# Performance work log

Measured on AMD Instinct MI355X. Metric: run time of the kernel, lower is better.

The kernel has to match this reference:

```python
import jax, jax.numpy as jnp
import numpy as np

B, N = 2, 6
H, W = 64, 64            # BEV grid
FH, FW = 32, 88          # camera feature map
DIM, FEAT_DIM = 128, 128
HEADS, DH = 4, 32
QW1, QW2 = 8, 8          # query window
KW1, KW2 = 4, 11         # key/val window
IMG_H, IMG_W = 224, 480
EPS = 1e-5


def _ln(t, g, b):
    m = t.mean(-1, keepdims=True)
    v = ((t - m) ** 2).mean(-1, keepdims=True)
    return (t - m) / jnp.sqrt(v + EPS) * g + b


def _bn_relu_conv(t, g, b, Wc):
    # eval-mode BatchNorm2d (running_mean=0, running_var=1) -> ReLU -> 1x1 conv
    y = jax.nn.relu(t / jnp.sqrt(1.0 + EPS) * g[:, None, None] + b[:, None, None])
    return jnp.einsum('oc,nchw->nohw', Wc, y)


def _normalize(t, axis):
    n = jnp.sqrt(jnp.sum(t * t, axis=axis, keepdims=True))
    return t / jnp.maximum(n, 1e-12)


def _win(t, w1, w2):
    # (..., X*w1, Y*w2, d) -> (..., X, Y, w1, w2, d)
    s = t.shape
    t = t.reshape(*s[:-3], s[-3] // w1, w1, s[-2] // w2, w2, s[-1])
    return jnp.swapaxes(t, -4, -3)


def _unwin(t):
    # (..., X, Y, w1, w2, d) -> (..., X*w1, Y*w2, d)
    s = t.shape
    return jnp.swapaxes(t, -4, -3).reshape(*s[:-5], s[-5] * s[-3], s[-4] * s[-2], s[-1])


def _gridwin(t, w1, w2):
    bb, nn, Ht, Wt, d = t.shape
    t = t.reshape(bb, nn, w1, Ht // w1, w2, Wt // w2, d)
    return t.transpose(0, 1, 3, 5, 2, 4, 6)  # (b, n, X, Y, w1, w2, d)


def _cross_win_attn(qw, kw, vw, ln_g, ln_b, Wqkv, bqkv, Wp, bp, skip):
    b, n, X, Y, w1, w2, d = qw.shape
    f1, f2 = kw.shape[4], kw.shape[5]
    L = X * Y
    q = qw.transpose(0, 2, 3, 1, 4, 5, 6).reshape(b, L, n * w1 * w2, d)
    k = kw.transpose(0, 2, 3, 1, 4, 5, 6).reshape(b, L, n * f1 * f2, d)
    v = vw.transpose(0, 2, 3, 1, 4, 5, 6).reshape(b, L, n * f1 * f2, d)
    q = _ln(q, ln_g[0], ln_b[0]) @ Wqkv[0] + bqkv[0]
    k = _ln(k, ln_g[1], ln_b[1]) @ Wqkv[1] + bqkv[1]
    v = _ln(v, ln_g[2], ln_b[2]) @ Wqkv[2] + bqkv[2]
    split = lambda t: t.reshape(*t.shape[:-1], HEADS, DH)  # head-major channel split
    q, k, v = split(q), split(k), split(v)
    att = jax.nn.softmax(DH ** -0.5 * jnp.einsum('blqhd,blkhd->bhlqk', q, k), axis=-1)
    o = jnp.einsum('bhlqk,blkhd->blqhd', att, v).reshape(b, L, n * w1 * w2, HEADS * DH)
    o = o @ Wp + bp
    o = o.reshape(b, X, Y, n, w1, w2, d).mean(3)  # mean over cameras
    return o + skip


def _forward(x, grid, feature, I_inv, E_inv,
             bn_fl_g, bn_fl_b, W_fl, bn_fp_g, bn_fp_b, W_fp,
             W_bev, b_bev, W_img, W_cam,
             attn_ln_g, attn_ln_b, attn_Wqkv, attn_bqkv, attn_Wp, attn_bp,
             pn_g, pn_b, Wma, bma, Wmb, bmb, post_g, post_b):
    b, n = feature.shape[:2]
    # image plane (buffer)
    xs = jnp.linspace(0.0, 1.0, FW) * IMG_W
    ys = jnp.linspace(0.0, 1.0, FH) * IMG_H
    gx, gy = jnp.meshgrid(xs, ys)  # (FH, FW) each
    plane = jnp.stack([gx, gy, jnp.ones_like(gx)], 0).reshape(3, FH * FW)
    # camera embedding from translation column of E_inv
    c = E_inv[..., -1]                                   # (b, n, 4)
    c_embed = jnp.einsum('oc,bnc->bno', W_cam, c)        # (b, n, dim)
    # unprojected rays
    cam = jnp.einsum('bnij,jk->bnik', I_inv, plane)      # (b, n, 3, HW)
    cam = jnp.concatenate([cam, jnp.ones_like(cam[:, :, :1])], 2)
    d = jnp.einsum('bnij,bnjk->bnik', E_inv, cam)        # (b, n, 4, HW)
    d_img = d.reshape(b, n, 4, FH, FW)
    d_embed = jnp.einsum('oc,bnchw->bnohw', W_img, d_img)
    img_embed = _normalize(d_embed - c_embed[..., None, None], axis=2)
    # BEV positional embedding
    w_embed = jnp.einsum('oc,chw->ohw', W_bev, grid[:2]) + b_bev[:, None, None]
    bev_embed = _normalize(w_embed[None, None] - c_embed[..., None, None], axis=2)  # (b,n,dim,H,W)
    feat = feature.reshape(b * n, FEAT_DIM, FH, FW)
    key_im = img_embed + _bn_relu_conv(feat, bn_fp_g, bn_fp_b, W_fp).reshape(b, n, DIM, FH, FW)
    val_im = _bn_relu_conv(feat, bn_fl_g, bn_fl_b, W_fl).reshape(b, n, DIM, FH, FW)
    query = bev_embed + x[:, None]                       # (b, n, dim, H, W)
    # channel-last
    q_im = query.transpose(0, 1, 3, 4, 2)
    k_im = key_im.transpose(0, 1, 3, 4, 2)
    v_im = val_im.transpose(0, 1, 3, 4, 2)
    x_im = x.transpose(0, 2, 3, 1)
    # stage 1: local windows
    qw = _win(q_im, QW1, QW2)
    kw = _win(k_im, KW1, KW2)
    vw = _win(v_im, KW1, KW2)
    o1 = _cross_win_attn(qw, kw, vw, attn_ln_g[0], attn_ln_b[0], attn_Wqkv[0],
                         attn_bqkv[0], attn_Wp[0], attn_bp[0], _win(x_im, QW1, QW2))
    q1 = _unwin(o1)                                      # (b, H, W, d)
    q1 = q1 + jax.nn.gelu(_ln(q1, pn_g[0], pn_b[0]) @ Wma[0] + bma[0], approximate=False) @ Wmb[0] + bmb[0]
    # stage 2: grid (swapped) windows
    qg = jnp.broadcast_to(q1[:, None], (b, n) + q1.shape[1:])
    o2 = _cross_win_attn(_win(qg, QW1, QW2), _gridwin(k_im, KW1, KW2), _gridwin(v_im, KW1, KW2),
                         attn_ln_g[1], attn_ln_b[1], attn_Wqkv[1], attn_bqkv[1],
                         attn_Wp[1], attn_bp[1], _win(q1, QW1, QW2))
    q2 = _unwin(o2)
    q2 = q2 + jax.nn.gelu(_ln(q2, pn_g[1], pn_b[1]) @ Wma[1] + bma[1], approximate=False) @ Wmb[1] + bmb[1]
    out = _ln(q2, post_g, post_b)
    return out.transpose(0, 3, 1, 2)                     # (b, dim, H, W)


def setup_inputs() -> dict:
    key = jax.random.key(0)
    ks = jax.random.split(key, 16)
    rn = lambda i, shape, sc=0.02: jax.random.normal(ks[i], shape, dtype=jnp.float32) * sc
    return {
        'index': 0,
        'x': jax.random.normal(ks[0], (B, DIM, H, W), dtype=jnp.float32),
        'grid': jax.random.normal(ks[1], (2, H, W), dtype=jnp.float32),
        'feature': jax.random.normal(ks[2], (B, N, FEAT_DIM, FH, FW), dtype=jnp.float32),
        'I_inv': jax.random.normal(ks[3], (B, N, 3, 3), dtype=jnp.float32),
        'E_inv': jax.random.normal(ks[4], (B, N, 4, 4), dtype=jnp.float32),
        'bn_fl_g': jnp.ones((FEAT_DIM,), jnp.float32), 'bn_fl_b': jnp.zeros((FEAT_DIM,), jnp.float32),
        'W_fl': rn(5, (DIM, FEAT_DIM)),
        'bn_fp_g': jnp.ones((FEAT_DIM,), jnp.float32), 'bn_fp_b': jnp.zeros((FEAT_DIM,), jnp.float32),
        'W_fp': rn(6, (DIM, FEAT_DIM)),
        'W_bev': rn(7, (DIM, 2)), 'b_bev': jnp.zeros((DIM,), jnp.float32),
        'W_img': rn(8, (DIM, 4)), 'W_cam': rn(9, (DIM, 4)),
        'attn_ln_g': jnp.ones((2, 3, DIM), jnp.float32), 'attn_ln_b': jnp.zeros((2, 3, DIM), jnp.float32),
        'attn_Wqkv': rn(10, (2, 3, DIM, HEADS * DH)), 'attn_bqkv': jnp.zeros((2, 3, HEADS * DH), jnp.float32),
        'attn_Wp': rn(11, (2, HEADS * DH, DIM)), 'attn_bp': jnp.zeros((2, DIM), jnp.float32),
        'pn_g': jnp.ones((2, DIM), jnp.float32), 'pn_b': jnp.zeros((2, DIM), jnp.float32),
        'Wma': rn(12, (2, DIM, 2 * DIM)), 'bma': jnp.zeros((2, 2 * DIM), jnp.float32),
        'Wmb': rn(13, (2, 2 * DIM, DIM)), 'bmb': jnp.zeros((2, DIM), jnp.float32),
        'post_g': jnp.ones((DIM,), jnp.float32), 'post_b': jnp.zeros((DIM,), jnp.float32),
    }


def reference(index, x, grid, feature, I_inv, E_inv,
              bn_fl_g, bn_fl_b, W_fl, bn_fp_g, bn_fp_b, W_fp,
              W_bev, b_bev, W_img, W_cam,
              attn_ln_g, attn_ln_b, attn_Wqkv, attn_bqkv, attn_Wp, attn_bp,
              pn_g, pn_b, Wma, bma, Wmb, bmb, post_g, post_b):
    del index  # grid for this index is passed directly
    return _forward(x, grid, feature, I_inv, E_inv,
                    bn_fl_g, bn_fl_b, W_fl, bn_fp_g, bn_fp_b, W_fp,
                    W_bev, b_bev, W_img, W_cam,
                    attn_ln_g, attn_ln_b, attn_Wqkv, attn_bqkv, attn_Wp, attn_bp,
                    pn_g, pn_b, Wma, bma, Wmb, bmb, post_g, post_b)
```

## Files before the change

### kernel.cpp

```cpp
#include <hip/hip_runtime.h>
#include <math.h>


typedef __attribute__((ext_vector_type(8))) short short8;
typedef __attribute__((ext_vector_type(4))) float f32x4;

__device__ __forceinline__ unsigned short f2bf(float f){
  union { float f; unsigned u; } v; v.f = f;
  unsigned r = v.u + 0x7FFF + ((v.u >> 16) & 1);
  return (unsigned short)(r >> 16);
}
__device__ __forceinline__ float bf2f(unsigned short h){
  union { unsigned u; float f; } v; v.u = ((unsigned)h) << 16; return v.f;
}
__device__ __forceinline__ void store_bf16x8(unsigned short* p, const float* v){
  union { short8 s8; unsigned short u[8]; } u;
  #pragma unroll
  for (int i=0;i<8;i++) u.u[i] = f2bf(v[i]);
  *(short8*)p = u.s8;
}

__device__ __forceinline__ float gelu_erf(float x){
  float z = x * 0.70710678118654752f;
  float a = fabsf(z);
  float t = 1.0f / fmaf(0.3275911f, a, 1.0f);
  float p = t*(0.254829592f + t*(-0.284496736f + t*(1.421413741f +
            t*(-1.453152027f + t*1.061405429f))));
  float er = 1.0f - p*__expf(-a*a);
  er = copysignf(er, z);
  return 0.5f * x * (1.0f + er);
}

__device__ __forceinline__ size_t remap_kv(int tok, int mode){
  int bn = tok / 2816; int p = tok - bn*2816;
  int b = bn / 6, n = bn - b*6;
  int i = p / 88, j = p - i*88;
  int l, t;
  if (mode == 1){
    int jw = j / 11;
    l = (i >> 2)*8 + jw;
    t = n*44 + (i & 3)*11 + (j - jw*11);
  } else {
    l = (i & 7)*8 + (j & 7);
    t = n*44 + (i >> 3)*11 + (j >> 3);
  }
  return (size_t)((b*64 + l)*264 + t);
}

__global__ __launch_bounds__(128) void k_prep(
    const float* __restrict__ qkv, const float* __restrict__ wp,
    const float* __restrict__ wma, const float* __restrict__ wmb,
    const float* __restrict__ wfl, const float* __restrict__ wfp,
    unsigned short* __restrict__ Wt,
    const float* __restrict__ Iinv, const float* __restrict__ Einv,
    const float* __restrict__ Wimg, const float* __restrict__ Wcam,
    unsigned short* __restrict__ K1h,
    const float* __restrict__ gridp, const float* __restrict__ Wbev,
    const float* __restrict__ bbev, const float* __restrict__ x,
    const float* __restrict__ lg, const float* __restrict__ lb,
    const float* __restrict__ abqkv, float* __restrict__ biasP,
    unsigned short* __restrict__ Qh){
  __shared__ float sx[128][9];
  int bid = blockIdx.x;
  if (bid < 64){
    const int sel[16]  = {0,0,0,0,0,0, 1,1, 2,2, 3,3,3,3, 4,5};
    const int soff[16] = {0,16384,32768,49152,65536,81920, 0,16384, 0,32768,
                          0,16384,32768,49152, 0,0};
    const int doff[16] = {0,16384,32768,49152,65536,81920, 98304,114688,
                          131072,163840, 196608,212992,229376,245760, 262144,278528};
    const int Ns[16]   = {128,128,128,128,128,128, 128,128, 256,256,
                          128,128,128,128, 128,128};
    const int trs[16]  = {1,1,1,1,1,1, 1,1, 1,1, 1,1,1,1, 0,0};
    int sg = bid >> 2, q = bid & 3;
    const float* srcs[6] = {qkv, wp, wma, wmb, wfl, wfp};
    const float* src = srcs[sel[sg]] + soff[sg];
    unsigned short* dst = Wt + doff[sg];
    int K = 128, N = Ns[sg];
    int quarter = (K*N) >> 2;
    bool fold = (sg >= 1 && sg <= 5);
    const float* gv = lg + sg*128;
    for (int idx = q*quarter + threadIdx.x; idx < (q+1)*quarter; idx += 128){
      int n = idx / K, k = idx - n*K;
      float v = trs[sg] ? src[k*N + n] : src[idx];
      if (fold) v *= gv[k];
      dst[idx] = f2bf(v);
    }
  } else if (bid < 70){
    int m = bid - 64;
    int n = threadIdx.x;
    float s = abqkv[m*128 + n];
    if (m > 0){
      const float* lnb = lb + m*128;
      const float* W = qkv + m*16384;
      for (int k=0;k<128;k++) s = fmaf(lnb[k], W[k*128 + n], s);
    }
    biasP[m*128 + n] = s;
  } else if (bid < 4294){
    int tile = bid - 70;
    int bn = tile / 352; int p0 = (tile - bn*352)*8;
    int xid = threadIdx.x >> 4, part = threadIdx.x & 15;
    int p = p0 + xid;
    int i = p / 88, j = p - i*88;
    float xs = (float)j * (480.0f/87.0f);
    float ys = (float)i * (224.0f/31.0f);
    const float* I = Iinv + bn*9;
    const float* E = Einv + bn*16;
    float c0 = I[0]*xs + I[1]*ys + I[2];
    float c1 = I[3]*xs + I[4]*ys + I[5];
    float c2 = I[6]*xs + I[7]*ys + I[8];
    float d0 = E[0]*c0 + E[1]*c1 + E[2]*c2 + E[3];
    float d1 = E[4]*c0 + E[5]*c1 + E[6]*c2 + E[7];
    float d2 = E[8]*c0 + E[9]*c1 + E[10]*c2 + E[11];
    float d3 = E[12]*c0 + E[13]*c1 + E[14]*c2 + E[15];
    float v[8]; float sq = 0.f;
    #pragma unroll
    for (int k=0;k<8;k++){
      int o = part*8 + k;
      const float* W = Wimg + o*4;
      const float* Wc = Wcam + o*4;
      float de = W[0]*d0 + W[1]*d1 + W[2]*d2 + W[3]*d3;
      float ce = Wc[0]*E[3] + Wc[1]*E[7] + Wc[2]*E[11] + Wc[3]*E[15];
      float vv = de - ce;
      v[k] = vv; sq = fmaf(vv, vv, sq);
    }
    #pragma unroll
    for (int off=8; off>0; off>>=1) sq += __shfl_xor(sq, off, 16);
    float rn = 1.0f / fmaxf(sqrtf(sq), 1e-12f);
    float o8[8];
    #pragma unroll
    for (int k=0;k<8;k++) o8[k] = v[k]*rn;
    store_bf16x8(K1h + (size_t)(bn*2816 + p)*128 + part*8, o8);
  } else {
    int bid2 = bid - 4294;
    int b = bid2 >> 9; int pp0 = (bid2 & 511) << 3;
    {
      int cg = threadIdx.x >> 3, px = threadIdx.x & 7;
      #pragma unroll
      for (int i=0;i<8;i++){
        int c = cg + 16*i;
        sx[c][px] = x[(size_t)b*524288 + (size_t)c*4096 + pp0 + px];
      }
    }
    __syncthreads();
    int xid = threadIdx.x >> 4, part = threadIdx.x & 15;
    int pix = pp0 + xid;
    int h = pix >> 6, w = pix & 63;
    int l = (h>>3)*8 + (w>>3);
    int tq = (h&7)*8 + (w&7);
    float g0 = gridp[pix], g1 = gridp[4096 + pix];
    float we[8], xv[8];
    #pragma unroll
    for (int k=0;k<8;k++){
      int o = part*8 + k;
      we[k] = Wbev[o*2]*g0 + Wbev[o*2+1]*g1 + bbev[o];
      xv[k] = sx[part*8+k][xid];
    }
    for (int n=0; n<6; n++){
      const float* E = Einv + (b*6+n)*16;
      float v[8]; float sq = 0.f;
      #pragma unroll
      for (int k=0;k<8;k++){
        int o = part*8 + k;
        const float* Wc = Wcam + o*4;
        float ce = Wc[0]*E[3] + Wc[1]*E[7] + Wc[2]*E[11] + Wc[3]*E[15];
        float vv = we[k] - ce;
        v[k] = vv; sq = fmaf(vv, vv, sq);
      }
      #pragma unroll
      for (int off=8; off>0; off>>=1) sq += __shfl_xor(sq, off, 16);
      float rn = 1.0f / fmaxf(sqrtf(sq), 1e-12f);
      float q[8]; float s=0.f, s2=0.f;
      #pragma unroll
      for (int k=0;k<8;k++){
        q[k] = fmaf(v[k], rn, xv[k]);
        s += q[k]; s2 = fmaf(q[k], q[k], s2);
      }
      #pragma unroll
      for (int off=8; off>0; off>>=1){ s += __shfl_xor(s, off, 16); s2 += __shfl_xor(s2, off, 16); }
      float mean = s*(1.f/128.f);
      float rstd = rsqrtf(fmaxf(s2*(1.f/128.f) - mean*mean, 0.f) + 1e-5f);
      size_t row = (size_t)((b*64 + l)*384 + n*64 + tq);
      float o8[8];
      #pragma unroll
      for (int k=0;k<8;k++){
        int c = part*8 + k;
        o8[k] = fmaf((q[k]-mean)*rstd, lg[c], lb[c]);
      }
      store_bf16x8(Qh + row*128 + part*8, o8);
    }
  }
}

__global__ __launch_bounds__(256) void k_conv(const float* __restrict__ feat,
    const float* __restrict__ gK, const float* __restrict__ bK,
    const unsigned short* __restrict__ WK, unsigned short* __restrict__ K1h,
    const float* __restrict__ gV, const float* __restrict__ bV,
    const unsigned short* __restrict__ WV, unsigned short* __restrict__ V1h){
  constexpr int KP_ = 136;
  __shared__ unsigned short sW[128*KP_];
  __shared__ unsigned short sA[128*KP_];
  __shared__ float sg[128], sb[128];
  __shared__ float sMean[128], sRstd[128];
  const int which = (blockIdx.x >= 264);
  const int bid = which ? blockIdx.x - 264 : blockIdx.x;
  const float* gg = which ? gV : gK;
  const float* bb = which ? bV : bK;
  const unsigned short* Wts = which ? WV : WK;
  unsigned short* OUT = which ? V1h : K1h;
  const int tid = threadIdx.x;
  const int base = bid * 128;
  for (int i = tid; i < 2048; i += 256){
    int n = i >> 4, k8 = (i & 15) << 3;
    *(short8*)&sW[n*KP_ + k8] = *(const short8*)(Wts + (size_t)n*128 + k8);
  }
  if (tid < 128){ sg[tid]=gg[tid]; sb[tid]=bb[tid]; }
  const float RSQ = rsqrtf(1.0f + 1e-5f);
  {
    int prow = tid & 127, cseg = tid >> 7;
    int bn = base / 2816;
    int p = base - bn*2816 + prow;
    const float* fb = feat + ((size_t)bn*128 + cseg*64)*2816 + p;
    #pragma unroll 8
    for (int i=0;i<64;i+=2){
      int c = cseg*64 + i;
      float t0 = fb[(size_t)i*2816] * RSQ;
      float t1 = fb[(size_t)(i+1)*2816] * RSQ;
      float y0 = fmaxf(fmaf(t0, sg[c],   sb[c]),   0.f);
      float y1 = fmaxf(fmaf(t1, sg[c+1], sb[c+1]), 0.f);
      unsigned u = (unsigned)f2bf(y0) | ((unsigned)f2bf(y1) << 16);
      *(unsigned*)&sA[prow*KP_ + c] = u;
    }
  }
  __syncthreads();
  const int lane = tid & 63, wv = tid >> 6;
  const int lane15 = lane & 15, quad = lane >> 4;
  const int n0 = wv * 32;
  f32x4 acc[8][2];
  #pragma unroll
  for (int mt=0; mt<8; mt++){ acc[mt][0]=(f32x4)0.f; acc[mt][1]=(f32x4)0.f; }
  const unsigned short* aptr = sA + lane15*KP_ + quad*8;
  const unsigned short* bptr = sW + (size_t)(n0 + lane15)*KP_ + quad*8;
  #pragma unroll
  for (int kk=0; kk<4; kk++){
    short8 af[8], bf2v[2];
    #pragma unroll
    for (int mt=0; mt<8; mt++) af[mt] = *(const short8*)(aptr + mt*16*KP_ + kk*32);
    bf2v[0] = *(const short8*)(bptr + kk*32);
    bf2v[1] = *(const short8*)(bptr + 16*KP_ + kk*32);
    #pragma unroll
    for (int mt=0; mt<8; mt++){
      acc[mt][0] = __builtin_amdgcn_mfma_f32_16x16x32_bf16(af[mt], bf2v[0], acc[mt][0], 0,0,0);
      acc[mt][1] = __builtin_amdgcn_mfma_f32_16x16x32_bf16(af[mt], bf2v[1], acc[mt][1], 0,0,0);
    }
  }
  __syncthreads();
  #pragma unroll
  for (int mt=0; mt<8; mt++){
    #pragma unroll
    for (int nt=0; nt<2; nt++){
      int col = n0 + nt*16 + lane15;
      #pragma unroll
      for (int r4=0; r4<4; r4++){
        int row = mt*16 + quad*4 + r4;
        float v = acc[mt][nt][r4];
        if (!which) v += bf2f(K1h[(size_t)(base+row)*128 + col]);
        sA[row*KP_ + col] = f2bf(v);
      }
    }
  }
  __syncthreads();
  {
    int r = tid >> 1, part = tid & 1;
    float s=0.f, s2=0.f;
    #pragma unroll 8
    for (int k=0;k<64;k++){
      float v = bf2f(sA[r*KP_ + part*64 + k]);
      s += v; s2 = fmaf(v,v,s2);
    }
    s += __shfl_xor(s, 1); s2 += __shfl_xor(s2, 1);
    if (part == 0){
      float mean = s*(1.f/128.f);
      sMean[r] = mean;
      sRstd[r] = rsqrtf(fmaxf(s2*(1.f/128.f) - mean*mean, 0.f) + 1e-5f);
    }
  }
  __syncthreads();
  for (int i = tid; i < 2048; i += 256){
    int row = i >> 4, seg = i & 15;
    float mean = sMean[row], rstd = sRstd[row];
    union { short8 s; unsigned short u[8]; } t;
    t.s = *(const short8*)&sA[row*KP_ + seg*8];
    float v[8];
    #pragma unroll
    for (int k=0;k<8;k++) v[k] = (bf2f(t.u[k]) - mean)*rstd;
    store_bf16x8(OUT + (size_t)(base+row)*128 + seg*8, v);
  }
}

struct GArg {
  const unsigned short* Xh;
  const unsigned short* Wt; const float* bias;
  unsigned short* OUTH; float oscale; int outmode;
};
struct G5 { GArg g[5]; int s[4]; };

__global__ __launch_bounds__(256) void k_qkv5(G5 A){
  constexpr int KP_ = 136;
  __shared__ unsigned short sW[128*KP_];
  __shared__ unsigned short sA[128*KP_];
  __shared__ float sbias[128];
  const int b0 = (int)blockIdx.x;
  const int ridx = (b0 < A.s[0]) ? 0 : (b0 < A.s[1]) ? 1 : (b0 < A.s[2]) ? 2
                 : (b0 < A.s[3]) ? 3 : 4;
  const GArg g = A.g[ridx];
  const int bid = b0 - (ridx ? A.s[ridx-1] : 0);
  const int base = bid * 128;
  const int tid = threadIdx.x;
  for (int i = tid; i < 2048; i += 256){
    int n = i >> 4, k8 = (i & 15) << 3;
    *(short8*)&sW[n*KP_ + k8] = *(const short8*)(g.Wt + (size_t)n*128 + k8);
  }
  if (tid < 128) sbias[tid] = g.bias[tid];
  {
    const int r = tid >> 1, part = tid & 1;
    const short8* src = (const short8*)(g.Xh + (size_t)(base+r)*128 + part*64);
    short8* dst = (short8*)(sA + r*KP_ + part*64);
    #pragma unroll
    for (int k=0;k<8;k++) dst[k] = src[k];
// ... 15 lines not shown
    bf2v[0] = *(const short8*)(bptr + kk*32);
    bf2v[1] = *(const short8*)(bptr + 16*KP_ + kk*32);
    #pragma unroll
    for (int mt=0; mt<8; mt++){
      acc[mt][0] = __builtin_amdgcn_mfma_f32_16x16x32_bf16(af[mt], bf2v[0], acc[mt][0], 0,0,0);
      acc[mt][1] = __builtin_amdgcn_mfma_f32_16x16x32_bf16(af[mt], bf2v[1], acc[mt][1], 0,0,0);
    }
  }
  __syncthreads();
  #pragma unroll
  for (int mt=0; mt<8; mt++){
    #pragma unroll
    for (int nt=0; nt<2; nt++){
      int col = n0 + nt*16 + lane15;
      float bsv = sbias[col];
      #pragma unroll
      for (int r4=0; r4<4; r4++){
        int row = mt*16 + quad*4 + r4;
        sA[row*KP_ + col] = f2bf((acc[mt][nt][r4] + bsv) * g.oscale);
      }
    }
  }
  __syncthreads();
  for (int i = tid; i < 2048; i += 256){
    int row = i >> 4, seg = i & 15;
    int rrow = base + row;
    size_t orow = g.outmode ? remap_kv(rrow, g.outmode) : (size_t)rrow;
    *(short8*)(g.OUTH + orow*128 + seg*8) = *(const short8*)&sA[row*KP_ + seg*8];
  }
}

__global__ __launch_bounds__(256) void k_tail(
    const unsigned short* __restrict__ AOh,
    const float* __restrict__ skipf, int skipmode,
    const unsigned short* __restrict__ WtP, const float* __restrict__ abp,
    const float* __restrict__ png, const float* __restrict__ pnb,
    const unsigned short* __restrict__ WtMAa, const unsigned short* __restrict__ WtMAb,
    const float* __restrict__ bma,
    const unsigned short* __restrict__ WtMBa, const unsigned short* __restrict__ WtMBb,
    const float* __restrict__ bmb,
    float* __restrict__ Q1out,
    const unsigned short* __restrict__ WtQ2, const float* __restrict__ q2bias,
    float q2scale, unsigned short* __restrict__ QPout,
    const float* __restrict__ postg, const float* __restrict__ postb,
    float* __restrict__ out){
  constexpr int KP_ = 136;
  __shared__ unsigned short sW[128*KP_];
  __shared__ unsigned short sX[32*KP_];
  __shared__ unsigned short sH1[32*KP_];
  __shared__ unsigned short sH2[32*KP_];
  __shared__ float sCUR[32*132];
  __shared__ float sbias[128];
  __shared__ float sg[128], sb2[128];
  __shared__ float sMean[32], sRstd[32];
  const int tid = threadIdx.x;
  const int base = blockIdx.x * 32;
  const int lane = tid & 63, wv = tid >> 6;
  const int lane15 = lane & 15, quad = lane >> 4;
  const int n0 = wv * 32;

  auto loadW = [&](const unsigned short* Wp){
    for (int i = tid; i < 2048; i += 256){
      int n = i >> 4, k8 = (i & 15) << 3;
      *(short8*)&sW[n*KP_ + k8] = *(const short8*)(Wp + (size_t)n*128 + k8);
    }
  };
  auto domfma = [&](const unsigned short* Asrc, f32x4 acc[2][2]){
    const unsigned short* aptr = Asrc + lane15*KP_ + quad*8;
    const unsigned short* bptr = sW + (size_t)(n0 + lane15)*KP_ + quad*8;
    #pragma unroll
    for (int kk=0; kk<4; kk++){
      short8 a0 = *(const short8*)(aptr + kk*32);
      short8 a1 = *(const short8*)(aptr + 16*KP_ + kk*32);
      short8 b0 = *(const short8*)(bptr + kk*32);
      short8 b1 = *(const short8*)(bptr + 16*KP_ + kk*32);
      acc[0][0] = __builtin_amdgcn_mfma_f32_16x16x32_bf16(a0,b0,acc[0][0],0,0,0);
      acc[1][0] = __builtin_amdgcn_mfma_f32_16x16x32_bf16(a1,b0,acc[1][0],0,0,0);
      acc[0][1] = __builtin_amdgcn_mfma_f32_16x16x32_bf16(a0,b1,acc[0][1],0,0,0);
      acc[1][1] = __builtin_amdgcn_mfma_f32_16x16x32_bf16(a1,b1,acc[1][1],0,0,0);
    }
  };

  loadW(WtP);
  {
    const int r = tid >> 3, part = tid & 7;
    const short8* src = (const short8*)(AOh + (size_t)(base+r)*128 + part*16);
    short8* dst = (short8*)(sX + r*KP_ + part*16);
    dst[0] = src[0]; dst[1] = src[1];
  }
  if (tid < 128){ sbias[tid] = abp[tid]; sg[tid] = png[tid]; sb2[tid] = pnb[tid]; }
  __syncthreads();
  {
    f32x4 acc[2][2];
    acc[0][0]=(f32x4)0.f; acc[0][1]=(f32x4)0.f;
    acc[1][0]=(f32x4)0.f; acc[1][1]=(f32x4)0.f;
    domfma(sX, acc);
    #pragma unroll
    for (int mt=0; mt<2; mt++)
      #pragma unroll
      for (int nt=0; nt<2; nt++){
        int col = n0 + nt*16 + lane15;
        float bsv = sbias[col];
        #pragma unroll
        for (int r4=0; r4<4; r4++){
          int row = mt*16 + quad*4 + r4;
          int rrow = base + row;
          float v = acc[mt][nt][r4] + bsv;
          if (skipmode == 1){
            int bb = rrow >> 12, l = (rrow >> 6) & 63, pp = rrow & 63;
            int pix = (((l>>3)*8 + (pp>>3)) << 6) + (l&7)*8 + (pp&7);
            v += skipf[(size_t)bb*524288 + (size_t)col*4096 + pix];
          } else {
            v += skipf[(size_t)rrow*128 + col];
          }
          sCUR[row*132 + col] = v;
        }
      }
// ... 179 lines not shown
      for (int off=4; off>0; off>>=1){ s += __shfl_xor(s, off, 8); s2 += __shfl_xor(s2, off, 8); }
      if (part == 0){
        float mean = s*(1.f/128.f);
        sMean[r] = mean;
        sRstd[r] = rsqrtf(fmaxf(s2*(1.f/128.f) - mean*mean, 0.f) + 1e-5f);
      }
    }
    __syncthreads();
    {
      int c = tid & 127, half = tid >> 7;
      int b = base >> 12, l = (base >> 6) & 63, p0 = base & 63;
      float go = postg[c], bo = postb[c];
      #pragma unroll
      for (int seg=0; seg<2; seg++){
        int p = p0 + half*16 + seg*8;
        int hrow = (l>>3)*8 + (p>>3);
        int w0 = (l&7)*8;
        float rr[8];
        #pragma unroll
        for (int j=0;j<8;j++){
          int row = half*16 + seg*8 + j;
          rr[j] = fmaf((sCUR[row*132 + c] - sMean[row])*sRstd[row], go, bo);
        }
        size_t obase = ((size_t)(b*128 + c))*4096 + (size_t)hrow*64 + w0;
        *(float4*)&out[obase]   = make_float4(rr[0],rr[1],rr[2],rr[3]);
        *(float4*)&out[obase+4] = make_float4(rr[4],rr[5],rr[6],rr[7]);
      }
    }
  }
}

__global__ __launch_bounds__(256) void k_attn2(const unsigned short* __restrict__ QPh,
    const unsigned short* __restrict__ KPh, const unsigned short* __restrict__ VPh,
    unsigned short* __restrict__ AOh, int nrep, int nQ){
  __shared__ unsigned short Ksh[288*40];
  __shared__ unsigned short Vt[32*296];
  __shared__ unsigned short Psh[4*16*40];
  __shared__ float rs[4*16];
  int hd = blockIdx.x & 3; int bl = blockIdx.x >> 2;
  size_t kvbase = (size_t)bl*264;
  int tid = threadIdx.x;
  for (int idx = tid; idx < 1056; idx += 256){
    int row = idx >> 2, seg = idx & 3;
    *(short8*)&Ksh[row*40 + seg*8] =
      *(const short8*)(KPh + (kvbase+row)*128 + hd*32 + seg*8);
  }
  for (int idx = tid; idx < 96; idx += 256){
    int row = 264 + (idx>>2), seg = idx & 3;
    short8 z = {0,0,0,0,0,0,0,0};
    *(short8*)&Ksh[row*40 + seg*8] = z;
  }
  for (int idx = tid; idx < 528; idx += 256){
    int kp = idx >> 2, seg = idx & 3;
    union { short8 s; unsigned short u[8]; } a, b;
    a.s = *(const short8*)(VPh + (kvbase + 2*kp)*128 + hd*32 + seg*8);
    b.s = *(const short8*)(VPh + (kvbase + 2*kp + 1)*128 + hd*32 + seg*8);
    #pragma unroll
    for (int i=0;i<8;i++)
      *(unsigned*)&Vt[(seg*8+i)*296 + 2*kp] = (unsigned)a.u[i] | ((unsigned)b.u[i] << 16);
  }
  for (int idx = tid; idx < 384; idx += 256){
    int d = idx / 12, kp = 264 + (idx % 12)*2;
    *(unsigned*)&Vt[d*296 + kp] = 0u;
  }
  __syncthreads();
  const int wv = tid >> 6, lane = tid & 63;
  const int lane15 = lane & 15, quad = lane >> 4;
  unsigned short* Pw = Psh + wv*640;
  float* rsw = rs + wv*16;
  short8 vfrag[9][2];
  #pragma unroll
  for (int kc=0; kc<9; kc++){
    vfrag[kc][0] = *(const short8*)&Vt[(lane15)*296      + kc*32 + quad*8];
    vfrag[kc][1] = *(const short8*)&Vt[(16+lane15)*296   + kc*32 + quad*8];
  }
  f32x4 macc0 = (f32x4)0.f, macc1 = (f32x4)0.f;
  for (int cam = 0; cam < nrep; cam++){
    int qrow = bl*nQ + (cam*4 + wv)*16 + lane15;
    short8 qf = *(const short8*)(QPh + (size_t)qrow*128 + hd*32 + quad*8);
    f32x4 oa0 = (f32x4)0.f, oa1 = (f32x4)0.f;
    float rsum = 0.f;
    #pragma unroll
    for (int kc=0; kc<9; kc++){
      #pragma unroll
      for (int sub=0; sub<2; sub++){
        int kt = kc*2 + sub;
        short8 kf = *(const short8*)&Ksh[(kt*16 + lane15)*40 + quad*8];
        f32x4 st = __builtin_amdgcn_mfma_f32_16x16x32_bf16(kf, qf, (f32x4)0.f, 0,0,0);
        int kbase = kt*16 + quad*4;
        float e0 = (kbase+0 < 264) ? __expf(st[0]) : 0.f;
        float e1 = (kbase+1 < 264) ? __expf(st[1]) : 0.f;
        float e2 = (kbase+2 < 264) ? __expf(st[2]) : 0.f;
        float e3 = (kbase+3 < 264) ? __expf(st[3]) : 0.f;
        rsum += (e0+e1)+(e2+e3);
        uint2 pk;
        pk.x = (unsigned)f2bf(e0) | ((unsigned)f2bf(e1) << 16);
        pk.y = (unsigned)f2bf(e2) | ((unsigned)f2bf(e3) << 16);
        *(uint2*)&Pw[lane15*40 + sub*16 + quad*4] = pk;
      }
      short8 pf = *(const short8*)&Pw[lane15*40 + quad*8];
      oa0 = __builtin_amdgcn_mfma_f32_16x16x32_bf16(pf, vfrag[kc][0], oa0, 0,0,0);
      oa1 = __builtin_amdgcn_mfma_f32_16x16x32_bf16(pf, vfrag[kc][1], oa1, 0,0,0);
    }
    rsum += __shfl_xor(rsum, 16);
    rsum += __shfl_xor(rsum, 32);
    if (lane < 16) rsw[lane] = rsum;
    f32x4 rv = *(f32x4*)&rsw[quad*4];
    #pragma unroll
    for (int r=0;r<4;r++){
      float inv = 1.f / rv[r];
      macc0[r] = fmaf(oa0[r], inv, macc0[r]);
      macc1[r] = fmaf(oa1[r], inv, macc1[r]);
    }
  }
  float sc = (nrep == 6) ? (1.f/6.f) : 1.f;
  int pixb = wv*16 + quad*4;
  #pragma unroll
  for (int r=0;r<4;r++){
    size_t rowo = ((size_t)(bl*64 + pixb + r))*128 + hd*32;
    AOh[rowo + lane15]      = f2bf(macc0[r]*sc);
    AOh[rowo + 16 + lane15] = f2bf(macc1[r]*sc);
  }
}

extern "C" void kernel_launch(void* const* d_in, const int* in_sizes, int n_in,
                              void* d_out, int out_size, void* d_ws, size_t ws_size,
                              hipStream_t stream) {
  (void)in_sizes; (void)n_in; (void)out_size; (void)ws_size;
  const float* x     = (const float*)d_in[1];
  const float* gridp = (const float*)d_in[2];
  const float* feat  = (const float*)d_in[3];
  const float* Iinv  = (const float*)d_in[4];
  const float* Einv  = (const float*)d_in[5];
  const float* gfl   = (const float*)d_in[6];
  const float* bfl   = (const float*)d_in[7];
  const float* Wfl   = (const float*)d_in[8];
  const float* gfp   = (const float*)d_in[9];
  const float* bfp   = (const float*)d_in[10];
  const float* Wfp   = (const float*)d_in[11];
  const float* Wbev  = (const float*)d_in[12];
  const float* bbev  = (const float*)d_in[13];
  const float* Wimg  = (const float*)d_in[14];
  const float* Wcam  = (const float*)d_in[15];
  const float* alng  = (const float*)d_in[16];
  const float* alnb  = (const float*)d_in[17];
  const float* aWqkv = (const float*)d_in[18];
  const float* abqkv = (const float*)d_in[19];
  const float* aWp   = (const float*)d_in[20];
  const float* abp   = (const float*)d_in[21];
  const float* png   = (const float*)d_in[22];
  const float* pnb   = (const float*)d_in[23];
  const float* Wma   = (const float*)d_in[24];
  const float* bma   = (const float*)d_in[25];
  const float* Wmb   = (const float*)d_in[26];
  const float* bmb   = (const float*)d_in[27];
  const float* postg = (const float*)d_in[28];
  const float* postb = (const float*)d_in[29];
  float* out = (float*)d_out;
  float* ws  = (float*)d_ws;
  const float QSC = 0.17677669529663687f;

  float* biasP = ws;
  unsigned short* Wt   = (unsigned short*)(ws + 2048);
  unsigned short* K1h  = (unsigned short*)(ws + 149504);
  unsigned short* V1h  = K1h + 4325376;
  unsigned short* KPh  = V1h + 4325376;
  unsigned short* VPh  = KPh + 4325376;
  unsigned short* KP2h = VPh + 4325376;
  unsigned short* VP2h = KP2h + 4325376;
  unsigned short* QPh  = VP2h + 4325376;
  unsigned short* Qbh  = QPh + 6291456;
  unsigned short* AOh  = Qbh + 6291456;
  float* Q1f = (float*)(AOh + 1048576);

  unsigned short* WtQ1 = Wt;            unsigned short* WtK1 = Wt + 16384;
  unsigned short* WtV1 = Wt + 32768;    unsigned short* WtQ2 = Wt + 49152;
  unsigned short* WtK2 = Wt + 65536;    unsigned short* WtV2 = Wt + 81920;
  unsigned short* WtP1 = Wt + 98304;    unsigned short* WtP2 = Wt + 114688;
  unsigned short* WtMA1 = Wt + 131072;  unsigned short* WtMA2 = Wt + 163840;
  unsigned short* WtMB1a = Wt + 196608; unsigned short* WtMB1b = Wt + 212992;
  unsigned short* WtMB2a = Wt + 229376; unsigned short* WtMB2b = Wt + 245760;
  unsigned short* WtFL = Wt + 262144;   unsigned short* WtFP = Wt + 278528;

  k_prep<<<5318, 128, 0, stream>>>(aWqkv, aWp, Wma, Wmb, Wfl, Wfp, Wt,
      Iinv, Einv, Wimg, Wcam, K1h, gridp, Wbev, bbev, x, alng, alnb,
      abqkv, biasP, Qbh);

  k_conv<<<528, 256, 0, stream>>>(feat, gfp, bfp, WtFP, K1h,
                                  gfl, bfl, WtFL, V1h);

  {
    G5 A;
    A.g[0] = GArg{Qbh, WtQ1, biasP,      QPh,  QSC, 0};
    A.g[1] = GArg{K1h, WtK1, biasP+128,  KPh,  1.f, 1};
    A.g[2] = GArg{V1h, WtV1, biasP+256,  VPh,  1.f, 1};
    A.g[3] = GArg{K1h, WtK2, biasP+512,  KP2h, 1.f, 2};
    A.g[4] = GArg{V1h, WtV2, biasP+640,  VP2h, 1.f, 2};
    A.s[0] = 384; A.s[1] = 648; A.s[2] = 912; A.s[3] = 1176;
    k_qkv5<<<1440, 256, 0, stream>>>(A);
  }
  k_attn2<<<512, 256, 0, stream>>>(QPh, KPh, VPh, AOh, 6, 384);
  k_tail<<<256, 256, 0, stream>>>(AOh, x, 1, WtP1, abp, png, pnb,
      WtMA1, WtMA1+16384, bma, WtMB1a, WtMB1b, bmb, Q1f,
      WtQ2, biasP+384, QSC, QPh,
      nullptr, nullptr, nullptr);
  k_attn2<<<512, 256, 0, stream>>>(QPh, KP2h, VP2h, AOh, 1, 64);
  k_tail<<<256, 256, 0, stream>>>(AOh, Q1f, 3, WtP2, abp+128, png+128, pnb+128,
      WtMA2, WtMA2+16384, bma+256, WtMB2a, WtMB2b, bmb+128, nullptr,
      nullptr, nullptr, 0.f, nullptr,
      postg, postb, out);
}
```

Before: 273.5 us.

## Split first cross-attention over camera groups with fp32 partials reduced in tail

The first attention launch is split into three camera groups of two cameras each, tripling the grid from 512 to 1536 blocks. Each group writes fp32 partial outputs to a new workspace buffer, and the first tail kernel sums the three partials before converting them to bf16. This targets low occupancy in the first attention pass, where only 512 blocks each looped over six cameras. In exchange, every group reloads the K/V tile into shared memory and writes extra fp32 traffic that the tail must read back.

```diff
diff --git a/kernel.cpp b/kernel.cpp
--- a/kernel.cpp
+++ b/kernel.cpp
@@ -375,6 +375,7 @@
 
 __global__ __launch_bounds__(256) void k_tail(
     const unsigned short* __restrict__ AOh,
+    const float* __restrict__ AOf3,
     const float* __restrict__ skipf, int skipmode,
     const unsigned short* __restrict__ WtP, const float* __restrict__ abp,
     const float* __restrict__ png, const float* __restrict__ pnb,
@@ -425,7 +426,16 @@
   };
 
   loadW(WtP);
-  {
+  if (AOf3){
+    const int r = tid >> 3, part = tid & 7;
+    const float* p0 = AOf3 + (size_t)(base+r)*128 + part*16;
+    float v[16];
+    #pragma unroll
+    for (int k=0;k<16;k++)
+      v[k] = p0[k] + p0[1048576 + k] + p0[2097152 + k];
+    store_bf16x8(sX + r*KP_ + part*16, v);
+    store_bf16x8(sX + r*KP_ + part*16 + 8, v+8);
+  } else {
     const int r = tid >> 3, part = tid & 7;
     const short8* src = (const short8*)(AOh + (size_t)(base+r)*128 + part*16);
     short8* dst = (short8*)(sX + r*KP_ + part*16);
@@ -671,12 +681,15 @@
 
 __global__ __launch_bounds__(256) void k_attn2(const unsigned short* __restrict__ QPh,
     const unsigned short* __restrict__ KPh, const unsigned short* __restrict__ VPh,
-    unsigned short* __restrict__ AOh, int nrep, int nQ){
+    unsigned short* __restrict__ AOh, float* __restrict__ AOf,
+    int ncam, int nQ, float osc){
   __shared__ unsigned short Ksh[288*40];
   __shared__ unsigned short Vt[32*296];
   __shared__ unsigned short Psh[4*16*40];
   __shared__ float rs[4*16];
-  int hd = blockIdx.x & 3; int bl = blockIdx.x >> 2;
+  int hd = blockIdx.x & 3; int bl = (blockIdx.x >> 2) & 127;
+  int cp = blockIdx.x >> 9;
+  int cam0 = cp * ncam;
   size_t kvbase = (size_t)bl*264;
   int tid = threadIdx.x;
   for (int idx = tid; idx < 1056; idx += 256){
@@ -714,7 +727,8 @@
     vfrag[kc][1] = *(const short8*)&Vt[(16+lane15)*296   + kc*32 + quad*8];
   }
   f32x4 macc0 = (f32x4)0.f, macc1 = (f32x4)0.f;
-  for (int cam = 0; cam < nrep; cam++){
+  for (int ci = 0; ci < ncam; ci++){
+    int cam = cam0 + ci;
     int qrow = bl*nQ + (cam*4 + wv)*16 + lane15;
     short8 qf = *(const short8*)(QPh + (size_t)qrow*128 + hd*32 + quad*8);
     f32x4 oa0 = (f32x4)0.f, oa1 = (f32x4)0.f;
@@ -752,13 +766,21 @@
       macc1[r] = fmaf(oa1[r], inv, macc1[r]);
     }
   }
-  float sc = (nrep == 6) ? (1.f/6.f) : 1.f;
   int pixb = wv*16 + quad*4;
-  #pragma unroll
-  for (int r=0;r<4;r++){
-    size_t rowo = ((size_t)(bl*64 + pixb + r))*128 + hd*32;
-    AOh[rowo + lane15]      = f2bf(macc0[r]*sc);
-    AOh[rowo + 16 + lane15] = f2bf(macc1[r]*sc);
+  if (AOf){
+    #pragma unroll
+    for (int r=0;r<4;r++){
+      size_t rowo = ((size_t)(cp*8192 + bl*64 + pixb + r))*128 + hd*32;
+      AOf[rowo + lane15]      = macc0[r]*osc;
+      AOf[rowo + 16 + lane15] = macc1[r]*osc;
+    }
+  } else {
+    #pragma unroll
+    for (int r=0;r<4;r++){
+      size_t rowo = ((size_t)(bl*64 + pixb + r))*128 + hd*32;
+      AOh[rowo + lane15]      = f2bf(macc0[r]*osc);
+      AOh[rowo + 16 + lane15] = f2bf(macc1[r]*osc);
+    }
   }
 }
 
@@ -811,6 +833,7 @@
   unsigned short* Qbh  = QPh + 6291456;
   unsigned short* AOh  = Qbh + 6291456;
   float* Q1f = (float*)(AOh + 1048576);
+  float* AOf = Q1f + 1048576;
 
   unsigned short* WtQ1 = Wt;            unsigned short* WtK1 = Wt + 16384;
   unsigned short* WtV1 = Wt + 32768;    unsigned short* WtQ2 = Wt + 49152;
@@ -838,13 +861,13 @@
     A.s[0] = 384; A.s[1] = 648; A.s[2] = 912; A.s[3] = 1176;
     k_qkv5<<<1440, 256, 0, stream>>>(A);
   }
-  k_attn2<<<512, 256, 0, stream>>>(QPh, KPh, VPh, AOh, 6, 384);
-  k_tail<<<256, 256, 0, stream>>>(AOh, x, 1, WtP1, abp, png, pnb,
+  k_attn2<<<1536, 256, 0, stream>>>(QPh, KPh, VPh, nullptr, AOf, 2, 384, 1.f/6.f);
+  k_tail<<<256, 256, 0, stream>>>(nullptr, AOf, x, 1, WtP1, abp, png, pnb,
       WtMA1, WtMA1+16384, bma, WtMB1a, WtMB1b, bmb, Q1f,
       WtQ2, biasP+384, QSC, QPh,
       nullptr, nullptr, nullptr);
-  k_attn2<<<512, 256, 0, stream>>>(QPh, KP2h, VP2h, AOh, 1, 64);
-  k_tail<<<256, 256, 0, stream>>>(AOh, Q1f, 3, WtP2, abp+128, png+128, pnb+128,
+  k_attn2<<<512, 256, 0, stream>>>(QPh, KP2h, VP2h, AOh, nullptr, 1, 64, 1.f);
+  k_tail<<<256, 256, 0, stream>>>(AOh, nullptr, Q1f, 3, WtP2, abp+128, png+128, pnb+128,
       WtMA2, WtMA2+16384, bma+256, WtMB2a, WtMB2b, bmb+128, nullptr,
       nullptr, nullptr, 0.f, nullptr,
       postg, postb, out);
```

Result: slower. 280.2 us (+2.4%).

## Merge prep and feature conv kernels, computing camera embedding inside conv blocks

Applied to the files above, without the earlier changes.

Fuses the preprocessing kernel and the 1x1 feature conv kernel into one launch. The conv blocks now convert fp32 conv weights to bf16 on the fly, and the key-path blocks compute the normalized image-direction embedding in shared memory. This removes a kernel launch and the global round trip of the K1h embedding. Q-prep blocks are widened to 256 threads handling 16 pixels each. The cost is more per-block work and redundant weight conversion in every conv block.

```diff
diff --git a/kernel.cpp b/kernel.cpp
--- a/kernel.cpp
+++ b/kernel.cpp
@@ -47,102 +47,82 @@
   return (size_t)((b*64 + l)*264 + t);
 }
 
-__global__ __launch_bounds__(128) void k_prep(
+__global__ __launch_bounds__(256) void k_prepconv(
     const float* __restrict__ qkv, const float* __restrict__ wp,
     const float* __restrict__ wma, const float* __restrict__ wmb,
-    const float* __restrict__ wfl, const float* __restrict__ wfp,
     unsigned short* __restrict__ Wt,
-    const float* __restrict__ Iinv, const float* __restrict__ Einv,
-    const float* __restrict__ Wimg, const float* __restrict__ Wcam,
-    unsigned short* __restrict__ K1h,
+    const float* __restrict__ abqkv, float* __restrict__ biasP,
     const float* __restrict__ gridp, const float* __restrict__ Wbev,
     const float* __restrict__ bbev, const float* __restrict__ x,
     const float* __restrict__ lg, const float* __restrict__ lb,
-    const float* __restrict__ abqkv, float* __restrict__ biasP,
-    unsigned short* __restrict__ Qh){
-  __shared__ float sx[128][9];
-  int bid = blockIdx.x;
-  if (bid < 64){
-    const int sel[16]  = {0,0,0,0,0,0, 1,1, 2,2, 3,3,3,3, 4,5};
-    const int soff[16] = {0,16384,32768,49152,65536,81920, 0,16384, 0,32768,
-                          0,16384,32768,49152, 0,0};
-    const int doff[16] = {0,16384,32768,49152,65536,81920, 98304,114688,
-                          131072,163840, 196608,212992,229376,245760, 262144,278528};
-    const int Ns[16]   = {128,128,128,128,128,128, 128,128, 256,256,
-                          128,128,128,128, 128,128};
-    const int trs[16]  = {1,1,1,1,1,1, 1,1, 1,1, 1,1,1,1, 0,0};
+    const float* __restrict__ Einv, const float* __restrict__ Wcam,
+    unsigned short* __restrict__ Qh,
+    const float* __restrict__ feat,
+    const float* __restrict__ gfp, const float* __restrict__ bfp,
+    const float* __restrict__ Wfp,
+    const float* __restrict__ gfl, const float* __restrict__ bfl,
+    const float* __restrict__ Wfl,
+    const float* __restrict__ Iinv, const float* __restrict__ Wimg,
+    unsigned short* __restrict__ K1h, unsigned short* __restrict__ V1h){
+  constexpr int KP_ = 136;
+  __shared__ unsigned short sW[128*KP_];
+  __shared__ unsigned short sA[128*KP_];
+  __shared__ float sg_[128], sb_[128];
+  __shared__ float sMean[128], sRstd[128], sRn[128];
+  __shared__ float sCE[128];
+  __shared__ float4 sWI4[128];
+  __shared__ float sIE[32];
+  const int bid = blockIdx.x;
+  const int tid = threadIdx.x;
+
+  if (bid < 56){
+    const int sel[14]  = {0,0,0,0,0,0, 1,1, 2,2, 3,3,3,3};
+    const int soff[14] = {0,16384,32768,49152,65536,81920, 0,16384, 0,32768,
+                          0,16384,32768,49152};
+    const int doff[14] = {0,16384,32768,49152,65536,81920, 98304,114688,
+                          131072,163840, 196608,212992,229376,245760};
+    const int Ns[14]   = {128,128,128,128,128,128, 128,128, 256,256,
+                          128,128,128,128};
     int sg = bid >> 2, q = bid & 3;
-    const float* srcs[6] = {qkv, wp, wma, wmb, wfl, wfp};
+    const float* srcs[4] = {qkv, wp, wma, wmb};
     const float* src = srcs[sel[sg]] + soff[sg];
     unsigned short* dst = Wt + doff[sg];
     int K = 128, N = Ns[sg];
     int quarter = (K*N) >> 2;
     bool fold = (sg >= 1 && sg <= 5);
     const float* gv = lg + sg*128;
-    for (int idx = q*quarter + threadIdx.x; idx < (q+1)*quarter; idx += 128){
+    for (int idx = q*quarter + tid; idx < (q+1)*quarter; idx += 256){
       int n = idx / K, k = idx - n*K;
-      float v = trs[sg] ? src[k*N + n] : src[idx];
+      float v = src[k*N + n];
       if (fold) v *= gv[k];
       dst[idx] = f2bf(v);
     }
-  } else if (bid < 70){
-    int m = bid - 64;
-    int n = threadIdx.x;
-    float s = abqkv[m*128 + n];
-    if (m > 0){
-      const float* lnb = lb + m*128;
-      const float* W = qkv + m*16384;
-      for (int k=0;k<128;k++) s = fmaf(lnb[k], W[k*128 + n], s);
-    }
-    biasP[m*128 + n] = s;
-  } else if (bid < 4294){
-    int tile = bid - 70;
-    int bn = tile / 352; int p0 = (tile - bn*352)*8;
-    int xid = threadIdx.x >> 4, part = threadIdx.x & 15;
-    int p = p0 + xid;
-    int i = p / 88, j = p - i*88;
-    float xs = (float)j * (480.0f/87.0f);
-    float ys = (float)i * (224.0f/31.0f);
-    const float* I = Iinv + bn*9;
-    const float* E = Einv + bn*16;
-    float c0 = I[0]*xs + I[1]*ys + I[2];
-    float c1 = I[3]*xs + I[4]*ys + I[5];
-    float c2 = I[6]*xs + I[7]*ys + I[8];
-    float d0 = E[0]*c0 + E[1]*c1 + E[2]*c2 + E[3];
-    float d1 = E[4]*c0 + E[5]*c1 + E[6]*c2 + E[7];
-    float d2 = E[8]*c0 + E[9]*c1 + E[10]*c2 + E[11];
-    float d3 = E[12]*c0 + E[13]*c1 + E[14]*c2 + E[15];
-    float v[8]; float sq = 0.f;
-    #pragma unroll
-    for (int k=0;k<8;k++){
-      int o = part*8 + k;
-      const float* W = Wimg + o*4;
-      const float* Wc = Wcam + o*4;
-      float de = W[0]*d0 + W[1]*d1 + W[2]*d2 + W[3]*d3;
-      float ce = Wc[0]*E[3] + Wc[1]*E[7] + Wc[2]*E[11] + Wc[3]*E[15];
-      float vv = de - ce;
-      v[k] = vv; sq = fmaf(vv, vv, sq);
-    }
-    #pragma unroll
-    for (int off=8; off>0; off>>=1) sq += __shfl_xor(sq, off, 16);
-    float rn = 1.0f / fmaxf(sqrtf(sq), 1e-12f);
-    float o8[8];
-    #pragma unroll
-    for (int k=0;k<8;k++) o8[k] = v[k]*rn;
-    store_bf16x8(K1h + (size_t)(bn*2816 + p)*128 + part*8, o8);
-  } else {
-    int bid2 = bid - 4294;
-    int b = bid2 >> 9; int pp0 = (bid2 & 511) << 3;
+  } else if (bid < 62){
+    if (tid < 128){
+      int m = bid - 56;
+      int n = tid;
+      float s = abqkv[m*128 + n];
+      if (m > 0){
+        const float* lnb = lb + m*128;
+        const float* W = qkv + m*16384;
+        for (int k=0;k<128;k++) s = fmaf(lnb[k], W[k*128 + n], s);
+      }
+      biasP[m*128 + n] = s;
+    }
+  } else if (bid < 574){
+    float* sx = (float*)sW;
+    int bid2 = bid - 62;
+    int b = bid2 >> 8; int pp0 = (bid2 & 255) << 4;
     {
-      int cg = threadIdx.x >> 3, px = threadIdx.x & 7;
+      int cg = tid >> 4, px = tid & 15;
       #pragma unroll
       for (int i=0;i<8;i++){
         int c = cg + 16*i;
-        sx[c][px] = x[(size_t)b*524288 + (size_t)c*4096 + pp0 + px];
-      }
-    }
-    __syncthreads();
-    int xid = threadIdx.x >> 4, part = threadIdx.x & 15;
+        sx[c*17 + px] = x[(size_t)b*524288 + (size_t)c*4096 + pp0 + px];
+      }
+    }
+    __syncthreads();
+    int xid = tid >> 4, part = tid & 15;
     int pix = pp0 + xid;
     int h = pix >> 6, w = pix & 63;
     int l = (h>>3)*8 + (w>>3);
@@ -153,7 +133,7 @@
     for (int k=0;k<8;k++){
       int o = part*8 + k;
       we[k] = Wbev[o*2]*g0 + Wbev[o*2+1]*g1 + bbev[o];
-      xv[k] = sx[part*8+k][xid];
+      xv[k] = sx[(part*8+k)*17 + xid];
     }
     for (int n=0; n<6; n++){
       const float* E = Einv + (b*6+n)*16;
@@ -188,112 +168,141 @@
       }
       store_bf16x8(Qh + row*128 + part*8, o8);
     }
-  }
-}
-
-__global__ __launch_bounds__(256) void k_conv(const float* __restrict__ feat,
-    const float* __restrict__ gK, const float* __restrict__ bK,
-    const unsigned short* __restrict__ WK, unsigned short* __restrict__ K1h,
-    const float* __restrict__ gV, const float* __restrict__ bV,
-    const unsigned short* __restrict__ WV, unsigned short* __restrict__ V1h){
-  constexpr int KP_ = 136;
-  __shared__ unsigned short sW[128*KP_];
-  __shared__ unsigned short sA[128*KP_];
-  __shared__ float sg[128], sb[128];
-  __shared__ float sMean[128], sRstd[128];
-  const int which = (blockIdx.x >= 264);
-  const int bid = which ? blockIdx.x - 264 : blockIdx.x;
-  const float* gg = which ? gV : gK;
-  const float* bb = which ? bV : bK;
-  const unsigned short* Wts = which ? WV : WK;
-  unsigned short* OUT = which ? V1h : K1h;
-  const int tid = threadIdx.x;
-  const int base = bid * 128;
-  for (int i = tid; i < 2048; i += 256){
-    int n = i >> 4, k8 = (i & 15) << 3;
-    *(short8*)&sW[n*KP_ + k8] = *(const short8*)(Wts + (size_t)n*128 + k8);
-  }
-  if (tid < 128){ sg[tid]=gg[tid]; sb[tid]=bb[tid]; }
-  const float RSQ = rsqrtf(1.0f + 1e-5f);
-  {
-    int prow = tid & 127, cseg = tid >> 7;
-    int bn = base / 2816;
-    int p = base - bn*2816 + prow;
-    const float* fb = feat + ((size_t)bn*128 + cseg*64)*2816 + p;
-    #pragma unroll 8
-    for (int i=0;i<64;i+=2){
-      int c = cseg*64 + i;
-      float t0 = fb[(size_t)i*2816] * RSQ;
-      float t1 = fb[(size_t)(i+1)*2816] * RSQ;
-      float y0 = fmaxf(fmaf(t0, sg[c],   sb[c]),   0.f);
-      float y1 = fmaxf(fmaf(t1, sg[c+1], sb[c+1]), 0.f);
-      unsigned u = (unsigned)f2bf(y0) | ((unsigned)f2bf(y1) << 16);
-      *(unsigned*)&sA[prow*KP_ + c] = u;
-    }
-  }
-  __syncthreads();
-  const int lane = tid & 63, wv = tid >> 6;
-  const int lane15 = lane & 15, quad = lane >> 4;
-  const int n0 = wv * 32;
-  f32x4 acc[8][2];
-  #pragma unroll
-  for (int mt=0; mt<8; mt++){ acc[mt][0]=(f32x4)0.f; acc[mt][1]=(f32x4)0.f; }
-  const unsigned short* aptr = sA + lane15*KP_ + quad*8;
-  const unsigned short* bptr = sW + (size_t)(n0 + lane15)*KP_ + quad*8;
-  #pragma unroll
-  for (int kk=0; kk<4; kk++){
-    short8 af[8], bf2v[2];
-    #pragma unroll
-    for (int mt=0; mt<8; mt++) af[mt] = *(const short8*)(aptr + mt*16*KP_ + kk*32);
-    bf2v[0] = *(const short8*)(bptr + kk*32);
-    bf2v[1] = *(const short8*)(bptr + 16*KP_ + kk*32);
+  } else {
+    const int bid2c = bid - 574;
+    const int which = (bid2c >= 264);
+    const int cbid = which ? bid2c - 264 : bid2c;
+    const float* gg = which ? gfl : gfp;
+    const float* bb = which ? bfl : bfp;
+    const float* Wf = which ? Wfl : Wfp;
+    unsigned short* OUT = which ? V1h : K1h;
+    const int base = cbid * 128;
+    const int bn = base / 2816;
+    const int pbase = base - bn*2816;
+    for (int i = tid; i < 2048; i += 256){
+      int n = i >> 4, k8 = (i & 15) << 3;
+      const float* wsp = Wf + (size_t)n*128 + k8;
+      float4 f0 = *(const float4*)wsp;
+      float4 f1 = *(const float4*)(wsp+4);
+      float v8[8] = {f0.x,f0.y,f0.z,f0.w,f1.x,f1.y,f1.z,f1.w};
+      store_bf16x8(&sW[n*KP_ + k8], v8);
+    }
+    if (tid < 128){ sg_[tid]=gg[tid]; sb_[tid]=bb[tid]; }
+    if (!which){
+      if (tid < 128){
+        const float* E = Einv + bn*16;
+        float4 wc = *(const float4*)(Wcam + tid*4);
+        sCE[tid] = wc.x*E[3] + wc.y*E[7] + wc.z*E[11] + wc.w*E[15];
+        sWI4[tid] = *(const float4*)(Wimg + tid*4);
+      }
+      if (tid < 25) sIE[tid] = (tid < 9) ? Iinv[bn*9 + tid] : Einv[bn*16 + (tid-9)];
+    }
+    const float RSQ = rsqrtf(1.0f + 1e-5f);
+    {
+      int prow = tid & 127, cseg = tid >> 7;
+      int p = pbase + prow;
+      const float* fb = feat + ((size_t)bn*128 + cseg*64)*2816 + p;
+      #pragma unroll 8
+      for (int i=0;i<64;i+=2){
+        int c = cseg*64 + i;
+        float t0 = fb[(size_t)i*2816] * RSQ;
+        float t1 = fb[(size_t)(i+1)*2816] * RSQ;
+        float y0 = fmaxf(fmaf(t0, sg_[c],   sb_[c]),   0.f);
+        float y1 = fmaxf(fmaf(t1, sg_[c+1], sb_[c+1]), 0.f);
+        unsigned u = (unsigned)f2bf(y0) | ((unsigned)f2bf(y1) << 16);
+        *(unsigned*)&sA[prow*KP_ + c] = u;
+      }
+    }
+    __syncthreads();
+    const int lane = tid & 63, wv = tid >> 6;
+    const int lane15 = lane & 15, quad = lane >> 4;
+    const int n0 = wv * 32;
+    f32x4 acc[8][2];
+    #pragma unroll
+    for (int mt=0; mt<8; mt++){ acc[mt][0]=(f32x4)0.f; acc[mt][1]=(f32x4)0.f; }
+    const unsigned short* aptr = sA + lane15*KP_ + quad*8;
+    const unsigned short* bptr = sW + (size_t)(n0 + lane15)*KP_ + quad*8;
+    #pragma unroll
+    for (int kk=0; kk<4; kk++){
+      short8 af[8], bf2v[2];
+      #pragma unroll
+      for (int mt=0; mt<8; mt++) af[mt] = *(const short8*)(aptr + mt*16*KP_ + kk*32);
+      bf2v[0] = *(const short8*)(bptr + kk*32);
+      bf2v[1] = *(const short8*)(bptr + 16*KP_ + kk*32);
+      #pragma unroll
+      for (int mt=0; mt<8; mt++){
+        acc[mt][0] = __builtin_amdgcn_mfma_f32_16x16x32_bf16(af[mt], bf2v[0], acc[mt][0], 0,0,0);
+        acc[mt][1] = __builtin_amdgcn_mfma_f32_16x16x32_bf16(af[mt], bf2v[1], acc[mt][1], 0,0,0);
+      }
+    }
+    __syncthreads();
+    if (!which){
+      const int r = tid >> 1, half = tid & 1;
+      int p = pbase + r;
+      int ii = p / 88, jj = p - ii*88;
+      float xs = (float)jj * (480.0f/87.0f);
+      float ys = (float)ii * (224.0f/31.0f);
+      float c0 = sIE[0]*xs + sIE[1]*ys + sIE[2];
+      float c1 = sIE[3]*xs + sIE[4]*ys + sIE[5];
+      float c2 = sIE[6]*xs + sIE[7]*ys + sIE[8];
+      float d0 = sIE[9]*c0  + sIE[10]*c1 + sIE[11]*c2 + sIE[12];
+      float d1 = sIE[13]*c0 + sIE[14]*c1 + sIE[15]*c2 + sIE[16];
+      float d2 = sIE[17]*c0 + sIE[18]*c1 + sIE[19]*c2 + sIE[20];
+      float d3 = sIE[21]*c0 + sIE[22]*c1 + sIE[23]*c2 + sIE[24];
+      float sq = 0.f;
+      #pragma unroll 8
+      for (int k=0;k<64;k++){
+        int c = half*64 + k;
+        float4 w = sWI4[c];
+        float de = w.x*d0 + w.y*d1 + w.z*d2 + w.w*d3 - sCE[c];
+        sA[r*KP_ + c] = f2bf(de);
+        sq = fmaf(de, de, sq);
+      }
+      sq += __shfl_xor(sq, 1);
+      if (half == 0) sRn[r] = 1.0f / fmaxf(sqrtf(sq), 1e-12f);
+    }
+    __syncthreads();
     #pragma unroll
     for (int mt=0; mt<8; mt++){
-      acc[mt][0] = __builtin_amdgcn_mfma_f32_16x16x32_bf16(af[mt], bf2v[0], acc[mt][0], 0,0,0);
-      acc[mt][1] = __builtin_amdgcn_mfma_f32_16x16x32_bf16(af[mt], bf2v[1], acc[mt][1], 0,0,0);
-    }
-  }
-  __syncthreads();
-  #pragma unroll
-  for (int mt=0; mt<8; mt++){
-    #pragma unroll
-    for (int nt=0; nt<2; nt++){
-      int col = n0 + nt*16 + lane15;
-      #pragma unroll
-      for (int r4=0; r4<4; r4++){
-        int row = mt*16 + quad*4 + r4;
-        float v = acc[mt][nt][r4];
-        if (!which) v += bf2f(K1h[(size_t)(base+row)*128 + col]);
-        sA[row*KP_ + col] = f2bf(v);
-      }
-    }
-  }
-  __syncthreads();
-  {
-    int r = tid >> 1, part = tid & 1;
-    float s=0.f, s2=0.f;
-    #pragma unroll 8
-    for (int k=0;k<64;k++){
-      float v = bf2f(sA[r*KP_ + part*64 + k]);
-      s += v; s2 = fmaf(v,v,s2);
-    }
-    s += __shfl_xor(s, 1); s2 += __shfl_xor(s2, 1);
-    if (part == 0){
-      float mean = s*(1.f/128.f);
-      sMean[r] = mean;
-      sRstd[r] = rsqrtf(fmaxf(s2*(1.f/128.f) - mean*mean, 0.f) + 1e-5f);
-    }
-  }
-  __syncthreads();
-  for (int i = tid; i < 2048; i += 256){
-    int row = i >> 4, seg = i & 15;
-    float mean = sMean[row], rstd = sRstd[row];
-    union { short8 s; unsigned short u[8]; } t;
-    t.s = *(const short8*)&sA[row*KP_ + seg*8];
-    float v[8];
-    #pragma unroll
-    for (int k=0;k<8;k++) v[k] = (bf2f(t.u[k]) - mean)*rstd;
-    store_bf16x8(OUT + (size_t)(base+row)*128 + seg*8, v);
+      #pragma unroll
+      for (int nt=0; nt<2; nt++){
+        int col = n0 + nt*16 + lane15;
+        #pragma unroll
+        for (int r4=0; r4<4; r4++){
+          int row = mt*16 + quad*4 + r4;
+          float v = acc[mt][nt][r4];
+          if (!which) v += bf2f(sA[row*KP_ + col]) * sRn[row];
+          sA[row*KP_ + col] = f2bf(v);
+        }
+      }
+    }
+    __syncthreads();
+    {
+      int r = tid >> 1, part = tid & 1;
+      float s=0.f, s2=0.f;
+      #pragma unroll 8
+      for (int k=0;k<64;k++){
+        float v = bf2f(sA[r*KP_ + part*64 + k]);
+        s += v; s2 = fmaf(v,v,s2);
+      }
+      s += __shfl_xor(s, 1); s2 += __shfl_xor(s2, 1);
+      if (part == 0){
+        float mean = s*(1.f/128.f);
+        sMean[r] = mean;
+        sRstd[r] = rsqrtf(fmaxf(s2*(1.f/128.f) - mean*mean, 0.f) + 1e-5f);
+      }
+    }
+    __syncthreads();
+    for (int i = tid; i < 2048; i += 256){
+      int row = i >> 4, seg = i & 15;
+      float mean = sMean[row], rstd = sRstd[row];
+      union { short8 s; unsigned short u[8]; } t;
+      t.s = *(const short8*)&sA[row*KP_ + seg*8];
+      float v[8];
+      #pragma unroll
+      for (int k=0;k<8;k++) v[k] = (bf2f(t.u[k]) - mean)*rstd;
+      store_bf16x8(OUT + (size_t)(base+row)*128 + seg*8, v);
+    }
   }
 }
 
@@ -819,14 +828,10 @@
   unsigned short* WtMA1 = Wt + 131072;  unsigned short* WtMA2 = Wt + 163840;
   unsigned short* WtMB1a = Wt + 196608; unsigned short* WtMB1b = Wt + 212992;
   unsigned short* WtMB2a = Wt + 229376; unsigned short* WtMB2b = Wt + 245760;
-  unsigned short* WtFL = Wt + 262144;   unsigned short* WtFP = Wt + 278528;
-
-  k_prep<<<5318, 128, 0, stream>>>(aWqkv, aWp, Wma, Wmb, Wfl, Wfp, Wt,
-      Iinv, Einv, Wimg, Wcam, K1h, gridp, Wbev, bbev, x, alng, alnb,
-      abqkv, biasP, Qbh);
-
-  k_conv<<<528, 256, 0, stream>>>(feat, gfp, bfp, WtFP, K1h,
-                                  gfl, bfl, WtFL, V1h);
+
+  k_prepconv<<<1102, 256, 0, stream>>>(aWqkv, aWp, Wma, Wmb, Wt,
+      abqkv, biasP, gridp, Wbev, bbev, x, alng, alnb, Einv, Wcam, Qbh,
+      feat, gfp, bfp, Wfp, gfl, bfl, Wfl, Iinv, Wimg, K1h, V1h);
 
   {
     G5 A;
```

Result: faster. 254.1 us (-7.1%).
